# Kernel tuning notes

Hardware: AMD Instinct MI355X
Metric: run time of the kernel (lower is better)

Reference implementation:

```python
import jax, jax.numpy as jnp
import numpy as np

BIT_WIDTH = 4
INT_MAX = 2.0 ** (BIT_WIDTH - 1) - 1.0  # narrow-range signed 4-bit: [-7, 7]
SCALE_MIN = 2e-16


def setup_inputs() -> dict:
    key = jax.random.key(0)
    kx, kw, kb = jax.random.split(key, 3)
    x = jax.random.normal(kx, (4, 2048, 4096), dtype=jnp.float32)
    weight = jax.random.normal(kw, (4096, 4096), dtype=jnp.float32) * 0.02
    bias_param = jax.random.normal(kb, (4096,), dtype=jnp.float32) * 0.01
    return {"x": x, "weight": weight, "bias_param": bias_param}


def reference(x, weight, bias_param):
    # Per-output-channel symmetric weight scale from abs-max statistics (Brevitas
    # Int8WeightPerTensorFloat with scaling_per_output_channel=True, bit_width=4,
    # narrow range -> int range [-7, 7]).
    absmax = jnp.max(jnp.abs(weight), axis=1, keepdims=True)          # [out, 1]
    scale = jnp.maximum(absmax, SCALE_MIN) / INT_MAX                   # [out, 1]
    w_int = jnp.round(jnp.clip(weight / scale, -INT_MAX, INT_MAX))     # round-half-even, like torch
    w_deq = w_int * scale                                              # dequantized 4-bit weight

    # IntBias: bias quantized with the (per-channel) weight scale, no clamping
    # (32-bit int range is never hit in practice).
    b_scale = scale[:, 0]                                              # [out]
    b_deq = jnp.round(bias_param / b_scale) * b_scale

    # Linear: y = x @ W_q^T + b_q
    return jnp.einsum('bsi,oi->bso', x, w_deq) + b_deq
```

## Files before the change

### kernel.cpp

```cpp
#include <hip/hip_runtime.h>
#include <hip/hip_bf16.h>
#include <stdint.h>

typedef _Float16 f16x8 __attribute__((ext_vector_type(8)));
typedef float    f32x4 __attribute__((ext_vector_type(4)));

#define QMAX 7.0f
#define QSCALE_MIN 2e-16f

#define M_DIM 8192
#define N_DIM 4096
#define K_DIM 4096

#define BM 128
#define BN 128
#define BK 32

#define XH_BYTES ((size_t)M_DIM * K_DIM * 2)
#define WH_BYTES ((size_t)N_DIM * K_DIM * 2)
#define SCALE_BYTES ((size_t)N_DIM * 4)

__global__ __launch_bounds__(256) void quant_weight_kernel(
    const float* __restrict__ w, const float* __restrict__ bias,
    _Float16* __restrict__ wh, float* __restrict__ scale_out,
    float* __restrict__ bdeq_out)
{
    const int row = blockIdx.x;
    const int t = threadIdx.x;
    const float* wr = w + (size_t)row * K_DIM;

    float4 v[4];
#pragma unroll
    for (int i = 0; i < 4; ++i)
        v[i] = reinterpret_cast<const float4*>(wr)[t * 4 + i];

    float m = 0.f;
#pragma unroll
    for (int i = 0; i < 4; ++i) {
        m = fmaxf(m, fabsf(v[i].x));
        m = fmaxf(m, fabsf(v[i].y));
        m = fmaxf(m, fabsf(v[i].z));
        m = fmaxf(m, fabsf(v[i].w));
    }
#pragma unroll
    for (int off = 32; off; off >>= 1)
        m = fmaxf(m, __shfl_xor(m, off, 64));

    __shared__ float wmax[4];
    if ((t & 63) == 0) wmax[t >> 6] = m;
    __syncthreads();
    float am = fmaxf(fmaxf(wmax[0], wmax[1]), fmaxf(wmax[2], wmax[3]));
    float scale = fmaxf(am, QSCALE_MIN) / QMAX;

    f16x8 q[2];
#pragma unroll
    for (int i = 0; i < 4; ++i) {
        float e[4] = { v[i].x, v[i].y, v[i].z, v[i].w };
#pragma unroll
        for (int j = 0; j < 4; ++j) {
            float d = e[j] / scale;
            d = fminf(QMAX, fmaxf(-QMAX, d));
            q[i >> 1][(i & 1) * 4 + j] = (_Float16)rintf(d);
        }
    }
    _Float16* __restrict__ dst = wh + (size_t)row * K_DIM + t * 16;
    *reinterpret_cast<f16x8*>(dst)     = q[0];
    *reinterpret_cast<f16x8*>(dst + 8) = q[1];

    if (t == 0) {
        scale_out[row] = scale;
        bdeq_out[row]  = rintf(bias[row] / scale) * scale;
    }
}

__global__ __launch_bounds__(256) void convert_x_kernel(
    const float* __restrict__ x, _Float16* __restrict__ xh, size_t n8)
{
    size_t i = (size_t)blockIdx.x * blockDim.x + threadIdx.x;
    size_t stride = (size_t)gridDim.x * blockDim.x;
    for (size_t c = i; c < n8; c += stride) {
        float4 a = reinterpret_cast<const float4*>(x)[c * 2];
        float4 b = reinterpret_cast<const float4*>(x)[c * 2 + 1];
        f16x8 h;
        h[0] = (_Float16)a.x; h[1] = (_Float16)a.y;
        h[2] = (_Float16)a.z; h[3] = (_Float16)a.w;
        h[4] = (_Float16)b.x; h[5] = (_Float16)b.y;
        h[6] = (_Float16)b.z; h[7] = (_Float16)b.w;
        reinterpret_cast<f16x8*>(xh)[c] = h;
    }
}

__global__ __launch_bounds__(256) void gemm_kernel(
    const _Float16* __restrict__ A, const _Float16* __restrict__ B,
    const float* __restrict__ scale, const float* __restrict__ bdeq,
    float* __restrict__ C)
{
    __shared__ _Float16 As[BM * BK];
    __shared__ _Float16 Bs[BN * BK];

    const int t = threadIdx.x;
    const int l = t & 63;
    const int w = t >> 6;

    const int nwg = gridDim.x;
    const int cpx = nwg >> 3;
    const int bid = blockIdx.x;
    const int swz = (bid & 7) * cpx + (bid >> 3);
    const int nbn = N_DIM / BN;
    const int bm = swz / nbn, bn = swz % nbn;

    const int wrow = w >> 1, wcol = w & 1;

    f32x4 acc[4][4] = {};

    const int e0 = t * 8;
    const int r0 = e0 >> 5, c0 = e0 & 31;
    const int e1 = (256 + t) * 8;
    const int r1 = e1 >> 5, c1 = e1 & 31;

    const _Float16* gA0 = A + ((size_t)(bm * BM + r0)) * K_DIM + c0;
    const _Float16* gA1 = A + ((size_t)(bm * BM + r1)) * K_DIM + c1;
    const _Float16* gB0 = B + ((size_t)(bn * BN + r0)) * K_DIM + c0;
    const _Float16* gB1 = B + ((size_t)(bn * BN + r1)) * K_DIM + c1;

    char* ldsA0 = (char*)As + w * 1024;
    char* ldsA1 = (char*)As + 4096 + w * 1024;
    char* ldsB0 = (char*)Bs + w * 1024;
    char* ldsB1 = (char*)Bs + 4096 + w * 1024;

    typedef __attribute__((address_space(1))) const void gvoid;
    typedef __attribute__((address_space(3))) void lvoid;

    for (int kt = 0; kt < K_DIM; kt += BK) {
        __builtin_amdgcn_global_load_lds((gvoid*)(gA0 + kt), (lvoid*)ldsA0, 16, 0, 0);
        __builtin_amdgcn_global_load_lds((gvoid*)(gA1 + kt), (lvoid*)ldsA1, 16, 0, 0);
        __builtin_amdgcn_global_load_lds((gvoid*)(gB0 + kt), (lvoid*)ldsB0, 16, 0, 0);
        __builtin_amdgcn_global_load_lds((gvoid*)(gB1 + kt), (lvoid*)ldsB1, 16, 0, 0);
        __syncthreads();

        f16x8 a[4], b[4];
#pragma unroll
        for (int i = 0; i < 4; ++i)
            a[i] = *reinterpret_cast<const f16x8*>(
                &As[(wrow * 64 + i * 16 + (l & 15)) * BK + (l >> 4) * 8]);
#pragma unroll
        for (int j = 0; j < 4; ++j)
            b[j] = *reinterpret_cast<const f16x8*>(
                &Bs[(wcol * 64 + j * 16 + (l & 15)) * BK + (l >> 4) * 8]);

#pragma unroll
        for (int i = 0; i < 4; ++i)
#pragma unroll
            for (int j = 0; j < 4; ++j)
                acc[i][j] = __builtin_amdgcn_mfma_f32_16x16x32_f16(
                    a[i], b[j], acc[i][j], 0, 0, 0);

        __syncthreads();
    }

    const int rowg = bm * BM + wrow * 64;
    const int colg = bn * BN + wcol * 64;
#pragma unroll
    for (int j = 0; j < 4; ++j) {
        const int n = colg + j * 16 + (l & 15);
        const float s = scale[n];
        const float bd = bdeq[n];
#pragma unroll
        for (int i = 0; i < 4; ++i) {
            const int mbase = rowg + i * 16 + (l >> 4) * 4;
#pragma unroll
            for (int r = 0; r < 4; ++r)
                C[(size_t)(mbase + r) * N_DIM + n] = acc[i][j][r] * s + bd;
        }
    }
}

__global__ __launch_bounds__(256) void scale_only_kernel(
    const float* __restrict__ w, const float* __restrict__ bias,
    float* __restrict__ scale_out, float* __restrict__ bdeq_out)
{
    const int row = blockIdx.x;
    const int t = threadIdx.x;
    const float* wr = w + (size_t)row * K_DIM;
    float m = 0.f;
#pragma unroll
    for (int i = 0; i < 4; ++i) {
        float4 v = reinterpret_cast<const float4*>(wr)[t * 4 + i];
        m = fmaxf(m, fmaxf(fmaxf(fabsf(v.x), fabsf(v.y)),
                           fmaxf(fabsf(v.z), fabsf(v.w))));
    }
#pragma unroll
    for (int off = 32; off; off >>= 1)
        m = fmaxf(m, __shfl_xor(m, off, 64));
    __shared__ float wmax[4];
    if ((t & 63) == 0) wmax[t >> 6] = m;
    __syncthreads();
    if (t == 0) {
        float am = fmaxf(fmaxf(wmax[0], wmax[1]), fmaxf(wmax[2], wmax[3]));
        float scale = fmaxf(am, QSCALE_MIN) / QMAX;
        scale_out[row] = scale;
        bdeq_out[row]  = rintf(bias[row] / scale) * scale;
    }
}

__global__ __launch_bounds__(256) void fallback_gemm(
    const float* __restrict__ x, const float* __restrict__ w,
    const float* __restrict__ scale, const float* __restrict__ bdeq,
    float* __restrict__ C)
{
    __shared__ float xs[32][33];
    __shared__ float wt[32][33];
    const int nbn = N_DIM / 32;
    const int bn = blockIdx.x % nbn, bm = blockIdx.x / nbn;
    const int tx = threadIdx.x & 31, ty = threadIdx.x >> 5;
    float acc[4] = {0.f, 0.f, 0.f, 0.f};
    for (int kt = 0; kt < K_DIM; kt += 32) {
        __syncthreads();
#pragma unroll
        for (int i = 0; i < 4; ++i) {
            int r = ty + i * 8;
            xs[r][tx] = x[(size_t)(bm * 32 + r) * K_DIM + kt + tx];
            float s = scale[bn * 32 + r];
            float wv = w[(size_t)(bn * 32 + r) * K_DIM + kt + tx];
            wt[r][tx] = rintf(fminf(QMAX, fmaxf(-QMAX, wv / s))) * s;
        }
        __syncthreads();
#pragma unroll 8
        for (int kk = 0; kk < 32; ++kk) {
            float wv = wt[tx][kk];
#pragma unroll
            for (int i = 0; i < 4; ++i)
                acc[i] = fmaf(xs[ty + i * 8][kk], wv, acc[i]);
        }
    }
    const float bd = bdeq[bn * 32 + tx];
#pragma unroll
    for (int i = 0; i < 4; ++i)
        C[(size_t)(bm * 32 + ty + i * 8) * N_DIM + bn * 32 + tx] = acc[i] + bd;
}

extern "C" void kernel_launch(void* const* d_in, const int* in_sizes, int n_in,
                              void* d_out, int out_size, void* d_ws, size_t ws_size,
                              hipStream_t stream)
{
    const float* x    = (const float*)d_in[0];
    const float* wgt  = (const float*)d_in[1];
    const float* bias = (const float*)d_in[2];
    float* out = (float*)d_out;

    char* ws = (char*)d_ws;

    if (ws_size >= XH_BYTES + WH_BYTES + 2 * SCALE_BYTES) {
        _Float16* xh   = (_Float16*)(ws);
        _Float16* wh   = (_Float16*)(ws + XH_BYTES);
        float* scale   = (float*)(ws + XH_BYTES + WH_BYTES);
        float* bdeq    = scale + N_DIM;

        quant_weight_kernel<<<N_DIM, 256, 0, stream>>>(wgt, bias, wh, scale, bdeq);
        convert_x_kernel<<<2048, 256, 0, stream>>>(x, xh, (size_t)M_DIM * K_DIM / 8);
        gemm_kernel<<<(M_DIM / BM) * (N_DIM / BN), 256, 0, stream>>>(
            xh, wh, scale, bdeq, out);
    } else {
        float* scale = (float*)ws;
        float* bdeq  = scale + N_DIM;
        scale_only_kernel<<<N_DIM, 256, 0, stream>>>(wgt, bias, scale, bdeq);
        fallback_gemm<<<(M_DIM / 32) * (N_DIM / 32), 256, 0, stream>>>(
            x, wgt, scale, bdeq, out);
    }
}
```

Baseline: 573.6 us.

## Rewrite GEMM as 256x256 tile, 8-wave double-buffered pipeline with swizzled LDS

```diff
diff --git a/kernel.cpp b/kernel.cpp
--- a/kernel.cpp
+++ b/kernel.cpp
@@ -3,6 +3,7 @@
 #include <stdint.h>
 
 typedef _Float16 f16x8 __attribute__((ext_vector_type(8)));
+typedef _Float16 f16x4 __attribute__((ext_vector_type(4)));
 typedef float    f32x4 __attribute__((ext_vector_type(4)));
 
 #define QMAX 7.0f
@@ -12,13 +13,17 @@
 #define N_DIM 4096
 #define K_DIM 4096
 
-#define BM 128
-#define BN 128
-#define BK 32
+#define NT 64
 
 #define XH_BYTES ((size_t)M_DIM * K_DIM * 2)
 #define WH_BYTES ((size_t)N_DIM * K_DIM * 2)
 #define SCALE_BYTES ((size_t)N_DIM * 4)
+
+typedef __attribute__((address_space(1))) const void gvoid;
+typedef __attribute__((address_space(3))) void lvoid;
+
+#define BAR()  asm volatile("s_barrier" ::: "memory")
+#define LGK0() asm volatile("s_waitcnt lgkmcnt(0)" ::: "memory")
 
 __global__ __launch_bounds__(256) void quant_weight_kernel(
     const float* __restrict__ w, const float* __restrict__ bias,
@@ -32,7 +37,7 @@
     float4 v[4];
 #pragma unroll
     for (int i = 0; i < 4; ++i)
-        v[i] = reinterpret_cast<const float4*>(wr)[t * 4 + i];
+        v[i] = reinterpret_cast<const float4*>(wr)[i * 256 + t];
 
     float m = 0.f;
 #pragma unroll
@@ -52,20 +57,18 @@
     float am = fmaxf(fmaxf(wmax[0], wmax[1]), fmaxf(wmax[2], wmax[3]));
     float scale = fmaxf(am, QSCALE_MIN) / QMAX;
 
-    f16x8 q[2];
 #pragma unroll
     for (int i = 0; i < 4; ++i) {
         float e[4] = { v[i].x, v[i].y, v[i].z, v[i].w };
+        f16x4 q;
 #pragma unroll
         for (int j = 0; j < 4; ++j) {
             float d = e[j] / scale;
             d = fminf(QMAX, fmaxf(-QMAX, d));
-            q[i >> 1][(i & 1) * 4 + j] = (_Float16)rintf(d);
+            q[j] = (_Float16)rintf(d);
         }
-    }
-    _Float16* __restrict__ dst = wh + (size_t)row * K_DIM + t * 16;
-    *reinterpret_cast<f16x8*>(dst)     = q[0];
-    *reinterpret_cast<f16x8*>(dst + 8) = q[1];
+        reinterpret_cast<f16x4*>(wh + (size_t)row * K_DIM)[i * 256 + t] = q;
+    }
 
     if (t == 0) {
         scale_out[row] = scale;
@@ -90,87 +93,163 @@
     }
 }
 
-__global__ __launch_bounds__(256) void gemm_kernel(
+__global__ __launch_bounds__(512, 2) void gemm_kernel(
     const _Float16* __restrict__ A, const _Float16* __restrict__ B,
     const float* __restrict__ scale, const float* __restrict__ bdeq,
     float* __restrict__ C)
 {
-    __shared__ _Float16 As[BM * BK];
-    __shared__ _Float16 Bs[BN * BK];
-
-    const int t = threadIdx.x;
-    const int l = t & 63;
-    const int w = t >> 6;
-
-    const int nwg = gridDim.x;
-    const int cpx = nwg >> 3;
+    __shared__ __attribute__((aligned(128))) char smem[131072];
+
+    const int tid = threadIdx.x;
+    const int l = tid & 63;
+    const int w = tid >> 6;
+    const int wm = w >> 2;
+    const int wn = w & 3;
+
     const int bid = blockIdx.x;
-    const int swz = (bid & 7) * cpx + (bid >> 3);
-    const int nbn = N_DIM / BN;
-    const int bm = swz / nbn, bn = swz % nbn;
-
-    const int wrow = w >> 1, wcol = w & 1;
-
-    f32x4 acc[4][4] = {};
-
-    const int e0 = t * 8;
-    const int r0 = e0 >> 5, c0 = e0 & 31;
-    const int e1 = (256 + t) * 8;
-    const int r1 = e1 >> 5, c1 = e1 & 31;
-
-    const _Float16* gA0 = A + ((size_t)(bm * BM + r0)) * K_DIM + c0;
-    const _Float16* gA1 = A + ((size_t)(bm * BM + r1)) * K_DIM + c1;
-    const _Float16* gB0 = B + ((size_t)(bn * BN + r0)) * K_DIM + c0;
-    const _Float16* gB1 = B + ((size_t)(bn * BN + r1)) * K_DIM + c1;
-
-    char* ldsA0 = (char*)As + w * 1024;
-    char* ldsA1 = (char*)As + 4096 + w * 1024;
-    char* ldsB0 = (char*)Bs + w * 1024;
-    char* ldsB1 = (char*)Bs + 4096 + w * 1024;
-
-    typedef __attribute__((address_space(1))) const void gvoid;
-    typedef __attribute__((address_space(3))) void lvoid;
-
-    for (int kt = 0; kt < K_DIM; kt += BK) {
-        __builtin_amdgcn_global_load_lds((gvoid*)(gA0 + kt), (lvoid*)ldsA0, 16, 0, 0);
-        __builtin_amdgcn_global_load_lds((gvoid*)(gA1 + kt), (lvoid*)ldsA1, 16, 0, 0);
-        __builtin_amdgcn_global_load_lds((gvoid*)(gB0 + kt), (lvoid*)ldsB0, 16, 0, 0);
-        __builtin_amdgcn_global_load_lds((gvoid*)(gB1 + kt), (lvoid*)ldsB1, 16, 0, 0);
-        __syncthreads();
-
-        f16x8 a[4], b[4];
-#pragma unroll
-        for (int i = 0; i < 4; ++i)
-            a[i] = *reinterpret_cast<const f16x8*>(
-                &As[(wrow * 64 + i * 16 + (l & 15)) * BK + (l >> 4) * 8]);
+    const int swz = (bid & 7) * 64 + (bid >> 3);
+    const int bm = swz >> 4;
+    const int bn = swz & 15;
+
+    const int lrow = l & 15;
+    const unsigned kofs = (unsigned)(((l >> 4) * 16) ^ ((l & 4) << 3));
+    const unsigned aOff = (unsigned)(wm * 16384 + lrow * 128) + kofs;
+    const unsigned bOff = 65536u +
+        (unsigned)((wn >> 1) * 16384 + (wn & 1) * 8192 + lrow * 128) + kofs;
+
+    const int tp = tid ^ (((tid >> 5) & 1) << 1);
+    const int rowq = tp >> 3;
+    const int colE = (tp & 7) * 8;
+    const _Float16* aSrc = A + (size_t)(bm * 256 + rowq) * K_DIM + colE;
+    const _Float16* bSrc = B + (size_t)(bn * 256 + rowq) * K_DIM + colE;
+    const unsigned wOfs = (unsigned)(w * 1024);
+
+    auto stage = [&](int s) {
+        int T = s >> 2;
+        if (T >= NT) return;
+        int part = s & 3;
+        int half = part & 1;
+        bool isB = part < 2;
+        const _Float16* src = (isB ? bSrc : aSrc)
+                              + (size_t)(half * 128) * K_DIM + T * 64;
+        unsigned dst = (isB ? 65536u : 0u) + (unsigned)((T & 1) * 32768)
+                       + (unsigned)(half * 16384) + wOfs;
+        __builtin_amdgcn_global_load_lds((gvoid*)src,
+                                         (lvoid*)(smem + dst), 16, 0, 0);
+        __builtin_amdgcn_global_load_lds((gvoid*)(src + (size_t)64 * K_DIM),
+                                         (lvoid*)(smem + dst + 8192), 16, 0, 0);
+    };
+
+    f32x4 acc[8][4];
+#pragma unroll
+    for (int i = 0; i < 8; ++i)
 #pragma unroll
         for (int j = 0; j < 4; ++j)
-            b[j] = *reinterpret_cast<const f16x8*>(
-                &Bs[(wcol * 64 + j * 16 + (l & 15)) * BK + (l >> 4) * 8]);
-
-#pragma unroll
-        for (int i = 0; i < 4; ++i)
-#pragma unroll
-            for (int j = 0; j < 4; ++j)
-                acc[i][j] = __builtin_amdgcn_mfma_f32_16x16x32_f16(
-                    a[i], b[j], acc[i][j], 0, 0, 0);
-
-        __syncthreads();
-    }
-
-    const int rowg = bm * BM + wrow * 64;
-    const int colg = bn * BN + wcol * 64;
+            acc[i][j] = (f32x4){0.f, 0.f, 0.f, 0.f};
+
+    f16x8 a[4][2], b[4][2];
+
+    stage(0); stage(1); stage(2); stage(3);
+    asm volatile("s_waitcnt vmcnt(4)" ::: "memory");
+    stage(4); stage(5); stage(6);
+    asm volatile("s_waitcnt vmcnt(6)" ::: "memory");
+    BAR();
+
+    for (int t = 0; t < NT; ++t) {
+        const unsigned dbuf = (unsigned)((t & 1) * 32768);
+        const int sb = 7 + 4 * t;
+
+#pragma unroll
+        for (int i = 0; i < 4; ++i)
+#pragma unroll
+            for (int kq = 0; kq < 2; ++kq)
+                a[i][kq] = *(const f16x8*)(smem + (aOff + dbuf
+                                + (unsigned)(i * 2048 + kq * 64)));
+#pragma unroll
+        for (int j = 0; j < 4; ++j)
+#pragma unroll
+            for (int kq = 0; kq < 2; ++kq)
+                b[j][kq] = *(const f16x8*)(smem + (bOff + dbuf
+                                + (unsigned)(j * 2048 + kq * 64)));
+        stage(sb);
+        BAR(); LGK0();
+        __builtin_amdgcn_s_setprio(1);
+#pragma unroll
+        for (int i = 0; i < 4; ++i)
+#pragma unroll
+            for (int j = 0; j < 2; ++j)
+#pragma unroll
+                for (int kq = 0; kq < 2; ++kq)
+                    acc[i][j] = __builtin_amdgcn_mfma_f32_16x16x32_f16(
+                        a[i][kq], b[j][kq], acc[i][j], 0, 0, 0);
+        __builtin_amdgcn_s_setprio(0);
+        BAR();
+
+        stage(sb + 1);
+        BAR(); LGK0();
+        __builtin_amdgcn_s_setprio(1);
+#pragma unroll
+        for (int i = 0; i < 4; ++i)
+#pragma unroll
+            for (int j = 2; j < 4; ++j)
+#pragma unroll
+                for (int kq = 0; kq < 2; ++kq)
+                    acc[i][j] = __builtin_amdgcn_mfma_f32_16x16x32_f16(
+                        a[i][kq], b[j][kq], acc[i][j], 0, 0, 0);
+        __builtin_amdgcn_s_setprio(0);
+        BAR();
+
+#pragma unroll
+        for (int i = 0; i < 4; ++i)
+#pragma unroll
+            for (int kq = 0; kq < 2; ++kq)
+                a[i][kq] = *(const f16x8*)(smem + (aOff + dbuf
+                                + (unsigned)(8192 + i * 2048 + kq * 64)));
+        stage(sb + 2);
+        BAR(); LGK0();
+        __builtin_amdgcn_s_setprio(1);
+#pragma unroll
+        for (int i = 0; i < 4; ++i)
+#pragma unroll
+            for (int j = 0; j < 2; ++j)
+#pragma unroll
+                for (int kq = 0; kq < 2; ++kq)
+                    acc[4 + i][j] = __builtin_amdgcn_mfma_f32_16x16x32_f16(
+                        a[i][kq], b[j][kq], acc[4 + i][j], 0, 0, 0);
+        __builtin_amdgcn_s_setprio(0);
+        BAR();
+
+        stage(sb + 3);
+        if (t < NT - 2) { asm volatile("s_waitcnt vmcnt(6)" ::: "memory"); }
+        else            { asm volatile("s_waitcnt vmcnt(0)" ::: "memory"); }
+        BAR();
+        __builtin_amdgcn_s_setprio(1);
+#pragma unroll
+        for (int i = 0; i < 4; ++i)
+#pragma unroll
+            for (int j = 2; j < 4; ++j)
+#pragma unroll
+                for (int kq = 0; kq < 2; ++kq)
+                    acc[4 + i][j] = __builtin_amdgcn_mfma_f32_16x16x32_f16(
+                        a[i][kq], b[j][kq], acc[4 + i][j], 0, 0, 0);
+        __builtin_amdgcn_s_setprio(0);
+        BAR();
+        __builtin_amdgcn_sched_barrier(0);
+    }
+
+    const int rowBase = bm * 256 + wm * 128 + (l >> 4) * 4;
+    const int colBase = bn * 256 + wn * 64 + (l & 15);
 #pragma unroll
     for (int j = 0; j < 4; ++j) {
-        const int n = colg + j * 16 + (l & 15);
+        const int n = colBase + j * 16;
         const float s = scale[n];
         const float bd = bdeq[n];
 #pragma unroll
-        for (int i = 0; i < 4; ++i) {
-            const int mbase = rowg + i * 16 + (l >> 4) * 4;
+        for (int ri = 0; ri < 8; ++ri) {
+            const int R = rowBase + (ri >> 2) * 64 + (ri & 3) * 16;
 #pragma unroll
             for (int r = 0; r < 4; ++r)
-                C[(size_t)(mbase + r) * N_DIM + n] = acc[i][j][r] * s + bd;
+                C[(size_t)(R + r) * N_DIM + n] = acc[ri][j][r] * s + bd;
         }
     }
 }
@@ -185,7 +264,7 @@
     float m = 0.f;
 #pragma unroll
     for (int i = 0; i < 4; ++i) {
-        float4 v = reinterpret_cast<const float4*>(wr)[t * 4 + i];
+        float4 v = reinterpret_cast<const float4*>(wr)[i * 256 + t];
         m = fmaxf(m, fmaxf(fmaxf(fabsf(v.x), fabsf(v.y)),
                            fmaxf(fabsf(v.z), fabsf(v.w))));
     }
@@ -257,8 +336,8 @@
         float* bdeq    = scale + N_DIM;
 
         quant_weight_kernel<<<N_DIM, 256, 0, stream>>>(wgt, bias, wh, scale, bdeq);
-        convert_x_kernel<<<2048, 256, 0, stream>>>(x, xh, (size_t)M_DIM * K_DIM / 8);
-        gemm_kernel<<<(M_DIM / BM) * (N_DIM / BN), 256, 0, stream>>>(
+        convert_x_kernel<<<4096, 256, 0, stream>>>(x, xh, (size_t)M_DIM * K_DIM / 8);
+        gemm_kernel<<<(M_DIM / 256) * (N_DIM / 256), 512, 0, stream>>>(
             xh, wh, scale, bdeq, out);
     } else {
         float* scale = (float*)ws;
```

After: 515.2 us. 1.11x faster.
